# Performance work log

Hardware: AMD Instinct MI355X
Metric: run time of the kernel (lower is better)

The kernel has to match this reference:

```python
import jax, jax.numpy as jnp
import numpy as np

BOOST_STRENGTH = 1.0  # init kwarg boostStrength (already >= 0)


def setup_inputs() -> dict:
    key = jax.random.key(0)
    k1, k2 = jax.random.split(key)
    x = jax.random.normal(k1, (8192, 4096), dtype=jnp.float32)
    # duty cycles are running fractions of activity, roughly around k/n
    dutyCycles = jax.random.uniform(k2, (4096,), dtype=jnp.float32) * 0.2
    return {"x": x, "dutyCycles": dutyCycles, "k": 409}


def reference(x, dutyCycles, k):
    n = x.shape[1]
    boost_strength = jnp.maximum(jnp.float32(BOOST_STRENGTH), 0.0)
    target_density = jnp.float32(k) / jnp.float32(n)
    # boostFactors = exp[(targetDensity - dutyCycle) * boostStrength]
    boost_factors = jnp.exp((target_density - dutyCycles) * boost_strength)  # [n]
    boosted = x * boost_factors  # [B, n]
    topk_vals, _ = jax.lax.top_k(boosted, k)  # [B, k]
    bottom = jnp.min(topk_vals, axis=1, keepdims=True)  # per-row k-th largest
    mask = (boosted >= bottom).astype(x.dtype)
    return x * mask
```

## Files before the change

### kernel.cpp

```cpp
#include <hip/hip_runtime.h>
#include <cstdint>
#include <cstddef>

#define N_COLS 4096
#define TPB 256
#define NCOPY 16
#define HSTRIDE 257

__global__ void boost_kernel(const float* __restrict__ dc,
                             const int* __restrict__ kp,
                             float* __restrict__ bf) {
    int i = blockIdx.x * blockDim.x + threadIdx.x;
    if (i < N_COLS) {
        float td = (float)kp[0] / (float)N_COLS;
        float arg = td - dc[i];
        bf[i] = (float)exp((double)arg);
    }
}

__device__ __forceinline__ uint32_t orderable(float f) {
    uint32_t u = __float_as_uint(f);
    return (u & 0x80000000u) ? ~u : (u | 0x80000000u);
}

__global__ __launch_bounds__(TPB) void kwinner_kernel(
    const float* __restrict__ x, const float* __restrict__ bf,
    const int* __restrict__ kp, float* __restrict__ out)
{
    __shared__ uint32_t s_hist[NCOPY * HSTRIDE];
    __shared__ uint32_t s_cnt[256];
    __shared__ uint32_t s_sel;

    const int tid = threadIdx.x;
    const size_t row = blockIdx.x;
    const float4* xr = (const float4*)(x + row * (size_t)N_COLS);
    const float4* br = (const float4*)bf;
    float4* orow = (float4*)(out + row * (size_t)N_COLS);

    float4 xv[4];
    uint32_t u[16];

    #pragma unroll
    for (int j = 0; j < 4; ++j) {
        float4 v = xr[tid + j * TPB];
        float4 b = br[tid + j * TPB];
        xv[j] = v;
        u[j * 4 + 0] = orderable(v.x * b.x);
        u[j * 4 + 1] = orderable(v.y * b.y);
        u[j * 4 + 2] = orderable(v.z * b.z);
        u[j * 4 + 3] = orderable(v.w * b.w);
    }

    uint32_t rem = (uint32_t)kp[0];
    uint32_t prefix = 0;
    const uint32_t pmasks[4] = {0u, 0xFF000000u, 0xFFFF0000u, 0xFFFFFF00u};

    for (int pass = 0; pass < 4; ++pass) {
        const int shift = 24 - pass * 8;
        for (int i = tid; i < NCOPY * HSTRIDE; i += TPB) s_hist[i] = 0;
        __syncthreads();

        const uint32_t pm = pmasks[pass];
        const uint32_t base = (uint32_t)(tid & (NCOPY - 1)) * HSTRIDE;
        #pragma unroll
        for (int e = 0; e < 16; ++e) {
            uint32_t uu = u[e];
            if (((uu ^ prefix) & pm) == 0u) {
                atomicAdd(&s_hist[base + ((uu >> shift) & 255u)], 1u);
            }
        }
        __syncthreads();

        uint32_t c = 0;
        #pragma unroll
        for (int cc = 0; cc < NCOPY; ++cc) c += s_hist[cc * HSTRIDE + tid];
        s_cnt[tid] = c;
        __syncthreads();

        if (tid < 64) {
            uint4 v = ((const uint4*)s_cnt)[tid];
            uint32_t s3 = v.w;
            uint32_t s2 = v.z + s3;
            uint32_t s1 = v.y + s2;
            uint32_t s0 = v.x + s1;
            uint32_t T = s0;
            #pragma unroll
            for (int off = 1; off < 64; off <<= 1) {
                uint32_t t = (uint32_t)__shfl_down((int)T, off, 64);
                if (tid + off < 64) T += t;
            }
            uint32_t Tex = T - s0;
            uint32_t S0 = Tex + s0, S1 = Tex + s1, S2 = Tex + s2, S3 = Tex + s3;
            int b = -1; uint32_t sn = 0;
            if (S3 >= rem)      { b = 3; sn = S3 - v.w; }
            else if (S2 >= rem) { b = 2; sn = S2 - v.z; }
            else if (S1 >= rem) { b = 1; sn = S1 - v.y; }
            else if (S0 >= rem) { b = 0; sn = S0 - v.x; }
            uint32_t packed = (b >= 0)
                ? (((uint32_t)(4 * tid + b + 1) << 16) | sn)
                : 0u;
            #pragma unroll
            for (int off = 1; off < 64; off <<= 1) {
                uint32_t o = (uint32_t)__shfl_xor((int)packed, off, 64);
                packed = packed > o ? packed : o;
            }
            if (tid == 0) s_sel = packed;
        }
        __syncthreads();

        uint32_t packed = s_sel;
        uint32_t d = (packed >> 16) - 1u;
        uint32_t sn = packed & 0xFFFFu;
        rem -= sn;
        prefix |= d << shift;
    }

    const uint32_t thr = prefix;
    #pragma unroll
    for (int j = 0; j < 4; ++j) {
        float4 v = xv[j];
        float4 o;
        o.x = (u[j * 4 + 0] >= thr) ? v.x : 0.0f;
        o.y = (u[j * 4 + 1] >= thr) ? v.y : 0.0f;
        o.z = (u[j * 4 + 2] >= thr) ? v.z : 0.0f;
        o.w = (u[j * 4 + 3] >= thr) ? v.w : 0.0f;
        orow[tid + j * TPB] = o;
    }
}

extern "C" void kernel_launch(void* const* d_in, const int* in_sizes, int n_in,
                              void* d_out, int out_size, void* d_ws, size_t ws_size,
                              hipStream_t stream) {
    const float* x  = (const float*)d_in[0];
    const float* dc = (const float*)d_in[1];
    const int*   kp = (const int*)d_in[2];
    float* out = (float*)d_out;
    float* bf  = (float*)d_ws;

    const int n    = in_sizes[1];
    const int rows = in_sizes[0] / n;

    boost_kernel<<<(n + TPB - 1) / TPB, TPB, 0, stream>>>(dc, kp, bf);
    kwinner_kernel<<<rows, TPB, 0, stream>>>(x, bf, kp, out);
}
```

Measured before the change: 233.8 us.

## Replace last two radix passes with wave-level bitwise select on compacted candidates

After two 8-bit histogram passes, elements matching the 16-bit prefix are compacted into a small shared buffer. A single wavefront then resolves the remaining 16 bits with ballot/popcount bisection, falling back to the histogram passes if more than 256 candidates survive. It also clears the histogram while reducing it instead of in a separate loop, computes the scan redundantly in every wave to drop one barrier per pass, and reloads x from global at the end instead of keeping it in registers. The aim is fewer barriers and shared-memory atomics, at the cost of a second read of x and 16 serial ballot steps.

```diff
diff --git a/kernel.cpp b/kernel.cpp
--- a/kernel.cpp
+++ b/kernel.cpp
@@ -6,6 +6,7 @@
 #define TPB 256
 #define NCOPY 16
 #define HSTRIDE 257
+#define CAND_CAP 256
 
 __global__ void boost_kernel(const float* __restrict__ dc,
                              const int* __restrict__ kp,
@@ -29,96 +30,132 @@
 {
     __shared__ uint32_t s_hist[NCOPY * HSTRIDE];
     __shared__ uint32_t s_cnt[256];
+    __shared__ uint32_t s_cand[CAND_CAP];
+    __shared__ uint32_t s_m2;
     __shared__ uint32_t s_sel;
 
     const int tid = threadIdx.x;
+    const int lane = tid & 63;
     const size_t row = blockIdx.x;
     const float4* xr = (const float4*)(x + row * (size_t)N_COLS);
     const float4* br = (const float4*)bf;
     float4* orow = (float4*)(out + row * (size_t)N_COLS);
 
-    float4 xv[4];
     uint32_t u[16];
-
     #pragma unroll
     for (int j = 0; j < 4; ++j) {
         float4 v = xr[tid + j * TPB];
         float4 b = br[tid + j * TPB];
-        xv[j] = v;
         u[j * 4 + 0] = orderable(v.x * b.x);
         u[j * 4 + 1] = orderable(v.y * b.y);
         u[j * 4 + 2] = orderable(v.z * b.z);
         u[j * 4 + 3] = orderable(v.w * b.w);
     }
 
+    for (int i = tid; i < NCOPY * HSTRIDE; i += TPB) s_hist[i] = 0;
+    if (tid == 0) s_m2 = 0;
+    __syncthreads();
+
     uint32_t rem = (uint32_t)kp[0];
     uint32_t prefix = 0;
-    const uint32_t pmasks[4] = {0u, 0xFF000000u, 0xFFFF0000u, 0xFFFFFF00u};
+    const uint32_t base = (uint32_t)(tid & (NCOPY - 1)) * HSTRIDE;
 
-    for (int pass = 0; pass < 4; ++pass) {
-        const int shift = 24 - pass * 8;
-        for (int i = tid; i < NCOPY * HSTRIDE; i += TPB) s_hist[i] = 0;
-        __syncthreads();
-
-        const uint32_t pm = pmasks[pass];
-        const uint32_t base = (uint32_t)(tid & (NCOPY - 1)) * HSTRIDE;
+    auto hist_pass = [&](int shift, uint32_t pm) {
         #pragma unroll
         for (int e = 0; e < 16; ++e) {
             uint32_t uu = u[e];
-            if (((uu ^ prefix) & pm) == 0u) {
+            if (((uu ^ prefix) & pm) == 0u)
                 atomicAdd(&s_hist[base + ((uu >> shift) & 255u)], 1u);
-            }
         }
         __syncthreads();
-
         uint32_t c = 0;
         #pragma unroll
-        for (int cc = 0; cc < NCOPY; ++cc) c += s_hist[cc * HSTRIDE + tid];
+        for (int cc = 0; cc < NCOPY; ++cc) {
+            int idx = cc * HSTRIDE + tid;
+            c += s_hist[idx];
+            s_hist[idx] = 0;
+        }
         s_cnt[tid] = c;
         __syncthreads();
+        uint4 v = ((const uint4*)s_cnt)[lane];
+        uint32_t s3 = v.w;
+        uint32_t s2 = v.z + s3;
+        uint32_t s1 = v.y + s2;
+        uint32_t s0 = v.x + s1;
+        uint32_t T = s0;
+        #pragma unroll
+        for (int off = 1; off < 64; off <<= 1) {
+            uint32_t t = (uint32_t)__shfl_down((int)T, off, 64);
+            if (lane + off < 64) T += t;
+        }
+        uint32_t Tex = T - s0;
+        uint32_t S0 = Tex + s0, S1 = Tex + s1, S2 = Tex + s2, S3 = Tex + s3;
+        int b = -1; uint32_t sn = 0;
+        if (S3 >= rem)      { b = 3; sn = S3 - v.w; }
+        else if (S2 >= rem) { b = 2; sn = S2 - v.z; }
+        else if (S1 >= rem) { b = 1; sn = S1 - v.y; }
+        else if (S0 >= rem) { b = 0; sn = S0 - v.x; }
+        uint32_t packed = (b >= 0)
+            ? (((uint32_t)(4 * lane + b + 1) << 16) | sn)
+            : 0u;
+        #pragma unroll
+        for (int off = 1; off < 64; off <<= 1) {
+            uint32_t o = (uint32_t)__shfl_xor((int)packed, off, 64);
+            packed = packed > o ? packed : o;
+        }
+        uint32_t d = (packed >> 16) - 1u;
+        sn = packed & 0xFFFFu;
+        rem -= sn;
+        prefix |= d << shift;
+    };
 
+    hist_pass(24, 0u);
+    hist_pass(16, 0xFF000000u);
+
+    #pragma unroll
+    for (int e = 0; e < 16; ++e) {
+        uint32_t uu = u[e];
+        if (((uu ^ prefix) & 0xFFFF0000u) == 0u) {
+            uint32_t pos = atomicAdd(&s_m2, 1u);
+            if (pos < CAND_CAP) s_cand[pos] = uu;
+        }
+    }
+    __syncthreads();
+
+    const uint32_t m2 = s_m2;
+    uint32_t thr;
+    if (m2 <= CAND_CAP) {
         if (tid < 64) {
-            uint4 v = ((const uint4*)s_cnt)[tid];
-            uint32_t s3 = v.w;
-            uint32_t s2 = v.z + s3;
-            uint32_t s1 = v.y + s2;
-            uint32_t s0 = v.x + s1;
-            uint32_t T = s0;
+            uint32_t inval = ~prefix;
+            uint32_t e0 = (lane       < m2) ? s_cand[lane      ] : inval;
+            uint32_t e1 = (lane + 64  < m2) ? s_cand[lane + 64 ] : inval;
+            uint32_t e2 = (lane + 128 < m2) ? s_cand[lane + 128] : inval;
+            uint32_t e3 = (lane + 192 < m2) ? s_cand[lane + 192] : inval;
+            uint32_t cur = 0;
             #pragma unroll
-            for (int off = 1; off < 64; off <<= 1) {
-                uint32_t t = (uint32_t)__shfl_down((int)T, off, 64);
-                if (tid + off < 64) T += t;
+            for (int bpos = 15; bpos >= 0; --bpos) {
+                uint32_t t = prefix | cur | (1u << bpos);
+                uint32_t mask = ~((1u << bpos) - 1u);
+                uint32_t c = (uint32_t)__popcll(__ballot(((e0 ^ t) & mask) == 0u))
+                           + (uint32_t)__popcll(__ballot(((e1 ^ t) & mask) == 0u))
+                           + (uint32_t)__popcll(__ballot(((e2 ^ t) & mask) == 0u))
+                           + (uint32_t)__popcll(__ballot(((e3 ^ t) & mask) == 0u));
+                if (c >= rem) cur |= (1u << bpos);
+                else          rem -= c;
             }
-            uint32_t Tex = T - s0;
-            uint32_t S0 = Tex + s0, S1 = Tex + s1, S2 = Tex + s2, S3 = Tex + s3;
-            int b = -1; uint32_t sn = 0;
-            if (S3 >= rem)      { b = 3; sn = S3 - v.w; }
-            else if (S2 >= rem) { b = 2; sn = S2 - v.z; }
-            else if (S1 >= rem) { b = 1; sn = S1 - v.y; }
-            else if (S0 >= rem) { b = 0; sn = S0 - v.x; }
-            uint32_t packed = (b >= 0)
-                ? (((uint32_t)(4 * tid + b + 1) << 16) | sn)
-                : 0u;
-            #pragma unroll
-            for (int off = 1; off < 64; off <<= 1) {
-                uint32_t o = (uint32_t)__shfl_xor((int)packed, off, 64);
-                packed = packed > o ? packed : o;
-            }
-            if (tid == 0) s_sel = packed;
+            if (tid == 0) s_sel = prefix | cur;
         }
         __syncthreads();
-
-        uint32_t packed = s_sel;
-        uint32_t d = (packed >> 16) - 1u;
-        uint32_t sn = packed & 0xFFFFu;
-        rem -= sn;
-        prefix |= d << shift;
+        thr = s_sel;
+    } else {
+        hist_pass(8, 0xFFFF0000u);
+        hist_pass(0, 0xFFFFFF00u);
+        thr = prefix;
     }
 
-    const uint32_t thr = prefix;
     #pragma unroll
     for (int j = 0; j < 4; ++j) {
-        float4 v = xv[j];
+        float4 v = xr[tid + j * TPB];
         float4 o;
         o.x = (u[j * 4 + 0] >= thr) ? v.x : 0.0f;
         o.y = (u[j * 4 + 1] >= thr) ? v.y : 0.0f;
```

New measurement: 238.2 us. No clear change (+1.9%).

## Prefilter top-k candidates by a fixed threshold before the radix select

Applied to the files above, without the earlier changes.

Each wave compacts elements whose boosted value is at least 1.1 into a shared candidate buffer of up to 1024 entries. The radix select then runs over this small set: two 8-bit histogram passes, a second compaction, then a ballot-based bitwise search over the low 16 bits inside a single wave. If the candidate count falls outside [k, CAP], the kernel falls back to the full 4-pass radix select, so results stay exact for any input. The histogram is also re-laid out with 8 interleaved copies per bin, and x is re-read from memory for the output instead of being kept in registers. The threshold suits the expected distribution of inputs. The gain depends on how often the fast path is taken, and the final pass adds an extra read of x.

```diff
diff --git a/kernel.cpp b/kernel.cpp
--- a/kernel.cpp
+++ b/kernel.cpp
@@ -4,8 +4,10 @@
 
 #define N_COLS 4096
 #define TPB 256
-#define NCOPY 16
-#define HSTRIDE 257
+#define NCOPY 8
+#define HSTR 12
+#define NHWORDS (256 * HSTR)
+#define CAP 1024
 
 __global__ void boost_kernel(const float* __restrict__ dc,
                              const int* __restrict__ kp,
@@ -27,98 +29,186 @@
     const float* __restrict__ x, const float* __restrict__ bf,
     const int* __restrict__ kp, float* __restrict__ out)
 {
-    __shared__ uint32_t s_hist[NCOPY * HSTRIDE];
+    __shared__ uint32_t s_hist[NHWORDS];
     __shared__ uint32_t s_cnt[256];
-    __shared__ uint32_t s_sel;
-
-    const int tid = threadIdx.x;
+    __shared__ uint32_t s_cand[CAP];
+    __shared__ uint32_t s_m, s_m2, s_sel;
+
+    const int tid  = threadIdx.x;
+    const int lane = tid & 63;
+    const uint32_t copy = (uint32_t)(lane & (NCOPY - 1));
     const size_t row = blockIdx.x;
     const float4* xr = (const float4*)(x + row * (size_t)N_COLS);
     const float4* br = (const float4*)bf;
     float4* orow = (float4*)(out + row * (size_t)N_COLS);
 
-    float4 xv[4];
     uint32_t u[16];
-
     #pragma unroll
     for (int j = 0; j < 4; ++j) {
         float4 v = xr[tid + j * TPB];
         float4 b = br[tid + j * TPB];
-        xv[j] = v;
         u[j * 4 + 0] = orderable(v.x * b.x);
         u[j * 4 + 1] = orderable(v.y * b.y);
         u[j * 4 + 2] = orderable(v.z * b.z);
         u[j * 4 + 3] = orderable(v.w * b.w);
     }
 
-    uint32_t rem = (uint32_t)kp[0];
+    {
+        uint4* h4 = (uint4*)s_hist;
+        uint4 z; z.x = z.y = z.z = z.w = 0u;
+        #pragma unroll
+        for (int j = 0; j < 3; ++j) h4[tid + j * TPB] = z;
+    }
+    if (tid == 0) { s_m = 0; s_m2 = 0; }
+    __syncthreads();
+
+    auto wave_scatter = [&](uint32_t val, bool pred, uint32_t* buf,
+                            uint32_t* counter, uint32_t cap) {
+        unsigned long long msk = __ballot(pred);
+        if (msk) {
+            int leader = __builtin_ctzll(msk);
+            uint32_t base = 0;
+            if (lane == leader) base = atomicAdd(counter, (uint32_t)__popcll(msk));
+            base = (uint32_t)__shfl((int)base, leader, 64);
+            if (pred) {
+                uint32_t off = __builtin_amdgcn_mbcnt_hi(
+                    (uint32_t)(msk >> 32),
+                    __builtin_amdgcn_mbcnt_lo((uint32_t)msk, 0));
+                uint32_t p = base + off;
+                if (p < cap) buf[p] = val;
+            }
+        }
+    };
+
+    const uint32_t T0 = 0xBF8CCCCDu;
+    #pragma unroll
+    for (int e = 0; e < 16; ++e)
+        wave_scatter(u[e], u[e] >= T0, s_cand, &s_m, CAP);
+    __syncthreads();
+
+    const uint32_t k = (uint32_t)kp[0];
+    const uint32_t m = s_m;
+    uint32_t rem = k;
     uint32_t prefix = 0;
-    const uint32_t pmasks[4] = {0u, 0xFF000000u, 0xFFFF0000u, 0xFFFFFF00u};
-
-    for (int pass = 0; pass < 4; ++pass) {
-        const int shift = 24 - pass * 8;
-        for (int i = tid; i < NCOPY * HSTRIDE; i += TPB) s_hist[i] = 0;
-        __syncthreads();
-
-        const uint32_t pm = pmasks[pass];
-        const uint32_t base = (uint32_t)(tid & (NCOPY - 1)) * HSTRIDE;
-        #pragma unroll
-        for (int e = 0; e < 16; ++e) {
-            uint32_t uu = u[e];
-            if (((uu ^ prefix) & pm) == 0u) {
-                atomicAdd(&s_hist[base + ((uu >> shift) & 255u)], 1u);
+    uint32_t thr;
+
+    auto reduce_bins = [&]() {
+        uint4 a  = *(const uint4*)&s_hist[tid * HSTR];
+        uint4 b2 = *(const uint4*)&s_hist[tid * HSTR + 4];
+        uint4 z; z.x = z.y = z.z = z.w = 0u;
+        *(uint4*)&s_hist[tid * HSTR]     = z;
+        *(uint4*)&s_hist[tid * HSTR + 4] = z;
+        s_cnt[tid] = a.x + a.y + a.z + a.w + b2.x + b2.y + b2.z + b2.w;
+    };
+
+    auto scan_digit = [&](uint32_t& remr) -> uint32_t {
+        uint4 v = ((const uint4*)s_cnt)[lane];
+        uint32_t s3 = v.w, s2 = v.z + s3, s1 = v.y + s2, s0 = v.x + s1;
+        uint32_t T = s0;
+        #pragma unroll
+        for (int off = 1; off < 64; off <<= 1) {
+            uint32_t t = (uint32_t)__shfl_down((int)T, off, 64);
+            if (lane + off < 64) T += t;
+        }
+        uint32_t Tex = T - s0;
+        uint32_t S0 = Tex + s0, S1 = Tex + s1, S2 = Tex + s2, S3 = Tex + s3;
+        int b = -1; uint32_t sn = 0;
+        if (S3 >= remr)      { b = 3; sn = S3 - v.w; }
+        else if (S2 >= remr) { b = 2; sn = S2 - v.z; }
+        else if (S1 >= remr) { b = 1; sn = S1 - v.y; }
+        else if (S0 >= remr) { b = 0; sn = S0 - v.x; }
+        uint32_t packed = (b >= 0)
+            ? (((uint32_t)(4 * lane + b + 1) << 16) | sn)
+            : 0u;
+        #pragma unroll
+        for (int off = 1; off < 64; off <<= 1) {
+            uint32_t o = (uint32_t)__shfl_xor((int)packed, off, 64);
+            packed = packed > o ? packed : o;
+        }
+        remr -= (packed & 0xFFFFu);
+        return (packed >> 16) - 1u;
+    };
+
+    if (m >= k && m <= CAP) {
+        uint32_t cv[4]; bool cp[4];
+        #pragma unroll
+        for (int j = 0; j < 4; ++j) {
+            uint32_t idx = (uint32_t)tid + j * TPB;
+            cp[j] = idx < m;
+            cv[j] = cp[j] ? s_cand[idx] : 0u;
+        }
+        #pragma unroll
+        for (int j = 0; j < 4; ++j)
+            if (cp[j]) atomicAdd(&s_hist[((cv[j] >> 24) & 255u) * HSTR + copy], 1u);
+        __syncthreads();
+        reduce_bins();
+        __syncthreads();
+        prefix = scan_digit(rem) << 24;
+
+        #pragma unroll
+        for (int j = 0; j < 4; ++j)
+            if (cp[j] && ((cv[j] ^ prefix) & 0xFF000000u) == 0u)
+                atomicAdd(&s_hist[((cv[j] >> 16) & 255u) * HSTR + copy], 1u);
+        __syncthreads();
+        reduce_bins();
+        __syncthreads();
+        prefix |= scan_digit(rem) << 16;
+
+        uint32_t* s_cand2 = s_hist;
+        #pragma unroll
+        for (int j = 0; j < 4; ++j)
+            wave_scatter(cv[j],
+                         cp[j] && ((cv[j] ^ prefix) & 0xFFFF0000u) == 0u,
+                         s_cand2, &s_m2, (uint32_t)NHWORDS);
+        __syncthreads();
+        const uint32_t m2 = s_m2;
+
+        if (tid < 64) {
+            uint32_t cv2[16];
+            #pragma unroll
+            for (int r = 0; r < 16; ++r) {
+                uint32_t idx = (uint32_t)(r * 64) + lane;
+                cv2[r] = (idx < m2) ? s_cand2[idx] : ~prefix;
             }
-        }
-        __syncthreads();
-
-        uint32_t c = 0;
-        #pragma unroll
-        for (int cc = 0; cc < NCOPY; ++cc) c += s_hist[cc * HSTRIDE + tid];
-        s_cnt[tid] = c;
-        __syncthreads();
-
-        if (tid < 64) {
-            uint4 v = ((const uint4*)s_cnt)[tid];
-            uint32_t s3 = v.w;
-            uint32_t s2 = v.z + s3;
-            uint32_t s1 = v.y + s2;
-            uint32_t s0 = v.x + s1;
-            uint32_t T = s0;
+            uint32_t cur = 0;
             #pragma unroll
-            for (int off = 1; off < 64; off <<= 1) {
-                uint32_t t = (uint32_t)__shfl_down((int)T, off, 64);
-                if (tid + off < 64) T += t;
+            for (int bpos = 15; bpos >= 0; --bpos) {
+                uint32_t t  = prefix | cur | (1u << bpos);
+                uint32_t mk = ~((1u << bpos) - 1u);
+                uint32_t c = 0;
+                #pragma unroll
+                for (int r = 0; r < 16; ++r)
+                    if ((uint32_t)(r * 64) < m2)
+                        c += (uint32_t)__popcll(__ballot(((cv2[r] ^ t) & mk) == 0u));
+                if (c >= rem) cur |= (1u << bpos);
+                else          rem -= c;
             }
-            uint32_t Tex = T - s0;
-            uint32_t S0 = Tex + s0, S1 = Tex + s1, S2 = Tex + s2, S3 = Tex + s3;
-            int b = -1; uint32_t sn = 0;
-            if (S3 >= rem)      { b = 3; sn = S3 - v.w; }
-            else if (S2 >= rem) { b = 2; sn = S2 - v.z; }
-            else if (S1 >= rem) { b = 1; sn = S1 - v.y; }
-            else if (S0 >= rem) { b = 0; sn = S0 - v.x; }
-            uint32_t packed = (b >= 0)
-                ? (((uint32_t)(4 * tid + b + 1) << 16) | sn)
-                : 0u;
+            if (tid == 0) s_sel = prefix | cur;
+        }
+        __syncthreads();
+        thr = s_sel;
+    } else {
+        const uint32_t pmasks[4] = {0u, 0xFF000000u, 0xFFFF0000u, 0xFFFFFF00u};
+        rem = k; prefix = 0;
+        #pragma unroll 1
+        for (int pass = 0; pass < 4; ++pass) {
+            const int shift = 24 - pass * 8;
+            const uint32_t pm = pmasks[pass];
             #pragma unroll
-            for (int off = 1; off < 64; off <<= 1) {
-                uint32_t o = (uint32_t)__shfl_xor((int)packed, off, 64);
-                packed = packed > o ? packed : o;
-            }
-            if (tid == 0) s_sel = packed;
-        }
-        __syncthreads();
-
-        uint32_t packed = s_sel;
-        uint32_t d = (packed >> 16) - 1u;
-        uint32_t sn = packed & 0xFFFFu;
-        rem -= sn;
-        prefix |= d << shift;
-    }
-
-    const uint32_t thr = prefix;
+            for (int e = 0; e < 16; ++e)
+                if (((u[e] ^ prefix) & pm) == 0u)
+                    atomicAdd(&s_hist[((u[e] >> shift) & 255u) * HSTR + copy], 1u);
+            __syncthreads();
+            reduce_bins();
+            __syncthreads();
+            prefix |= scan_digit(rem) << shift;
+        }
+        thr = prefix;
+    }
+
     #pragma unroll
     for (int j = 0; j < 4; ++j) {
-        float4 v = xv[j];
+        float4 v = xr[tid + j * TPB];
         float4 o;
         o.x = (u[j * 4 + 0] >= thr) ? v.x : 0.0f;
         o.y = (u[j * 4 + 1] >= thr) ? v.y : 0.0f;
```

Measured after the change: 241.2 us. 1.03x slower.
